# Performance work log

Hardware: AMD Instinct MI355X
Metric: run time of the kernel (lower is better)

Reference implementation:

```python
import jax, jax.numpy as jnp
import numpy as np

B, K, D, H, ZDIM = 65536, 16, 64, 128, 16

def setup_inputs() -> dict:
    key = jax.random.key(0)
    ks = jax.random.split(key, 20)
    s = 0.05
    inp = {
        'z': jax.random.normal(ks[0], (B, ZDIM), dtype=jnp.float32),
        'y': jax.random.randint(ks[1], (B,), 0, K),
        # backbone: 4 fc blocks (Linear+ReLU)
        'bw0': jax.random.normal(ks[2], (ZDIM, H), dtype=jnp.float32) * s,
        'bb0': jnp.zeros((H,), dtype=jnp.float32),
        'bw1': jax.random.normal(ks[3], (H, H), dtype=jnp.float32) * s,
        'bb1': jnp.zeros((H,), dtype=jnp.float32),
        'bw2': jax.random.normal(ks[4], (H, H), dtype=jnp.float32) * s,
        'bb2': jnp.zeros((H,), dtype=jnp.float32),
        'bw3': jax.random.normal(ks[5], (H, H), dtype=jnp.float32) * s,
        'bb3': jnp.zeros((H,), dtype=jnp.float32),
        # K heads, weights stacked on leading expert axis; layers 0-2 have ReLU, layer 3 does not
        'hw0': jax.random.normal(ks[6], (K, H, H), dtype=jnp.float32) * s,
        'hb0': jnp.zeros((K, H), dtype=jnp.float32),
        'hw1': jax.random.normal(ks[7], (K, H, H), dtype=jnp.float32) * s,
        'hb1': jnp.zeros((K, H), dtype=jnp.float32),
        'hw2': jax.random.normal(ks[8], (K, H, H), dtype=jnp.float32) * s,
        'hb2': jnp.zeros((K, H), dtype=jnp.float32),
        'hw3': jax.random.normal(ks[9], (K, H, D), dtype=jnp.float32) * s,
        'hb3': jnp.zeros((K, D), dtype=jnp.float32),
    }
    return inp

def reference(z, y, bw0, bb0, bw1, bb1, bw2, bb2, bw3, bb3,
              hw0, hb0, hw1, hb1, hw2, hb2, hw3, hb3):
    h = jax.nn.relu(z @ bw0 + bb0)
    h = jax.nn.relu(h @ bw1 + bb1)
    h = jax.nn.relu(h @ bw2 + bb2)
    h = jax.nn.relu(h @ bw3 + bb3)          # [B, H]
    # all K expert heads (faithful to original: compute all, then gather)
    a = jax.nn.relu(jnp.einsum('bi,kij->bkj', h, hw0) + hb0)  # [B, K, H]
    a = jax.nn.relu(jnp.einsum('bki,kij->bkj', a, hw1) + hb1)
    a = jax.nn.relu(jnp.einsum('bki,kij->bkj', a, hw2) + hb2)
    a = jnp.einsum('bki,kij->bkj', a, hw3) + hb3              # [B, K, D], no ReLU
    # select the y-th head per sample
    out = jnp.take_along_axis(a, y[:, None, None], axis=1)[:, 0, :]  # [B, D]
    return out
```

## Files before the change

### kernel.cpp

```cpp
#include <hip/hip_runtime.h>
#include <hip/hip_bf16.h>
#include <stdint.h>


typedef _Float16 f16;
typedef __attribute__((ext_vector_type(2)))  _Float16 f16x2;
typedef __attribute__((ext_vector_type(8)))  _Float16 f16x8;
typedef __attribute__((ext_vector_type(16))) float    f32x16;
typedef uint32_t u32;
typedef __attribute__((ext_vector_type(2))) u32 u32x2;
typedef __attribute__((ext_vector_type(4))) u32 u32x4;

#define MFMA(a, b, c) __builtin_amdgcn_mfma_f32_32x32x16_f16((a), (b), (c), 0, 0, 0)

constexpr int Bc = 65536;
constexpr int Kc = 16;
constexpr int Hc = 128;
constexpr int Dc = 64;

constexpr int CAP  = 4608;
constexpr int SPB  = 32;
constexpr int BPE  = CAP / SPB;
constexpr int NBLK = Kc * BPE;
constexpr int NXCD = 8;
constexpr int CHUNK = NBLK / NXCD;

constexpr int BBW_F16 = 2048 + 3 * 16384;
constexpr int HWE_F16 = 3 * 16384 + 8192;

constexpr int PREP_BLKS = 52 + Kc * 56;

struct Act { f16x8 w[8]; };

__device__ __forceinline__ f32x16 zero16() {
    f32x16 z;
#pragma unroll
    for (int i = 0; i < 16; ++i) z[i] = 0.0f;
    return z;
}

template<bool RELU>
__device__ __forceinline__ void build_windows(
    const f32x16& c, const float4* bq, f16x8& w0, f16x8& w1)
{
    u32 P[8];
#pragma unroll
    for (int g = 0; g < 4; ++g) {
        const float bb[4] = {bq[g].x, bq[g].y, bq[g].z, bq[g].w};
        f16 h[4];
#pragma unroll
        for (int j = 0; j < 4; ++j) {
            float v = c[4 * g + j] + bb[j];
            if (RELU) v = fmaxf(v, 0.0f);
            h[j] = (f16)v;
        }
        f16x2 p0; p0[0] = h[0]; p0[1] = h[1];
        f16x2 p1; p1[0] = h[2]; p1[1] = h[3];
        P[2 * g]     = __builtin_bit_cast(u32, p0);
        P[2 * g + 1] = __builtin_bit_cast(u32, p1);
    }
    const u32x2 r02 = __builtin_amdgcn_permlane32_swap(P[0], P[2], false, false);
    const u32x2 r13 = __builtin_amdgcn_permlane32_swap(P[1], P[3], false, false);
    const u32x2 r46 = __builtin_amdgcn_permlane32_swap(P[4], P[6], false, false);
    const u32x2 r57 = __builtin_amdgcn_permlane32_swap(P[5], P[7], false, false);
    u32x4 W0 = { r02[0], r13[0], r02[1], r13[1] };
    u32x4 W1 = { r46[0], r57[0], r46[1], r57[1] };
    w0 = __builtin_bit_cast(f16x8, W0);
    w1 = __builtin_bit_cast(f16x8, W1);
}

__device__ __forceinline__ void layer_glb(
    const f16* __restrict__ gW, const float* __restrict__ biasG,
    const Act& src, Act& dst, int lane, int bh)
{
#pragma unroll
    for (int q = 0; q < 4; ++q) {
        const f16* pw = gW + q * 4096 + lane * 8;
        float4 bq[4];
#pragma unroll
        for (int g = 0; g < 4; ++g)
            bq[g] = *(const float4*)(biasG + 32 * q + 8 * g + 4 * bh);

        f32x16 c0 = zero16(), c1 = zero16();
        __builtin_amdgcn_s_setprio(1);
#pragma unroll
        for (int ks = 0; ks < 8; ++ks) {
            const f16x8 wh = *(const f16x8*)(pw + ks * 512);
            if (ks & 1) c1 = MFMA(wh, src.w[ks], c1);
            else        c0 = MFMA(wh, src.w[ks], c0);
        }
        __builtin_amdgcn_s_setprio(0);
        const f32x16 cs = c0 + c1;
        build_windows<true>(cs, bq, dst.w[2 * q], dst.w[2 * q + 1]);
    }
}

__device__ __forceinline__ void layer_final(
    const f16* __restrict__ gW, const float* __restrict__ biasG,
    const Act& src, float* __restrict__ out, int bidx, int lane, int bh)
{
#pragma unroll
    for (int q = 0; q < 2; ++q) {
        const f16* pw = gW + q * 4096 + lane * 8;
        float4 bq[4];
#pragma unroll
        for (int g = 0; g < 4; ++g)
            bq[g] = *(const float4*)(biasG + 32 * q + 8 * g + 4 * bh);

        f32x16 c0 = zero16(), c1 = zero16();
        __builtin_amdgcn_s_setprio(1);
#pragma unroll
        for (int ks = 0; ks < 8; ++ks) {
            const f16x8 wh = *(const f16x8*)(pw + ks * 512);
            if (ks & 1) c1 = MFMA(wh, src.w[ks], c1);
            else        c0 = MFMA(wh, src.w[ks], c0);
        }
        __builtin_amdgcn_s_setprio(0);
        if (bidx >= 0) {
            const f32x16 cs = c0 + c1;
#pragma unroll
            for (int g = 0; g < 4; ++g) {
                float4 v;
                v.x = cs[4 * g + 0] + bq[g].x;
                v.y = cs[4 * g + 1] + bq[g].y;
                v.z = cs[4 * g + 2] + bq[g].z;
                v.w = cs[4 * g + 3] + bq[g].w;
                *(float4*)(out + (size_t)bidx * Dc + 32 * q + 8 * g + 4 * bh) = v;
            }
        }
    }
}

__global__ __launch_bounds__(64, 2) void fused_mlp(
    const float* __restrict__ z,
    const int* __restrict__ idxb, const int* __restrict__ cursor,
    const f16* __restrict__ bbW,
    const float* __restrict__ bb0, const float* __restrict__ bb1,
    const float* __restrict__ bb2, const float* __restrict__ bb3,
    const f16* __restrict__ hW,
    const float* __restrict__ hb0, const float* __restrict__ hb1,
    const float* __restrict__ hb2, const float* __restrict__ hb3,
    float* __restrict__ out)
{
    const int blk = (blockIdx.x % NXCD) * CHUNK + blockIdx.x / NXCD;
    const int e = blk / BPE;
    const int local0 = (blk % BPE) * SPB;
    const int cnt = min(cursor[e * 16], CAP);
    if (cnt - local0 <= 0) return;

    const int lane = threadIdx.x & 63;
    const int l31 = lane & 31, bh = lane >> 5;

    int bidx = -1;
    const int sIdx = local0 + l31;
    if (sIdx < cnt) bidx = idxb[e * CAP + sIdx];

    f16x8 zw;
    if (bidx >= 0) {
        const float4 u0 = *(const float4*)(z + (size_t)bidx * 16 + bh * 8);
        const float4 u1 = *(const float4*)(z + (size_t)bidx * 16 + bh * 8 + 4);
        zw[0] = (f16)u0.x; zw[1] = (f16)u0.y; zw[2] = (f16)u0.z; zw[3] = (f16)u0.w;
        zw[4] = (f16)u1.x; zw[5] = (f16)u1.y; zw[6] = (f16)u1.z; zw[7] = (f16)u1.w;
    } else {
#pragma unroll
        for (int j = 0; j < 8; ++j) zw[j] = (f16)0.0f;
    }

    Act aA, aB;
#pragma unroll
    for (int q = 0; q < 4; ++q) {
        float4 bq[4];
#pragma unroll
        for (int g = 0; g < 4; ++g)
            bq[g] = *(const float4*)(bb0 + 32 * q + 8 * g + 4 * bh);
        const f16x8 wh = *(const f16x8*)(bbW + q * 512 + lane * 8);
        f32x16 c0 = zero16();
        c0 = MFMA(wh, zw, c0);
        build_windows<true>(c0, bq, aA.w[2 * q], aA.w[2 * q + 1]);
    }

    const size_t we = (size_t)e * HWE_F16;
    layer_glb(bbW + 2048,      bb1,          aA, aB, lane, bh);
    layer_glb(bbW + 18432,     bb2,          aB, aA, lane, bh);
    layer_glb(bbW + 34816,     bb3,          aA, aB, lane, bh);
    layer_glb(hW + we,         hb0 + e * Hc, aB, aA, lane, bh);
    layer_glb(hW + we + 16384, hb1 + e * Hc, aA, aB, lane, bh);
    layer_glb(hW + we + 32768, hb2 + e * Hc, aB, aA, lane, bh);
    layer_final(hW + we + 49152, hb3 + e * Dc, aA, out, bidx, lane, bh);
}

__global__ void prep_scatter(
    const float* __restrict__ bw0, const float* __restrict__ bw1,
    const float* __restrict__ bw2, const float* __restrict__ bw3,
    const float* __restrict__ hw0, const float* __restrict__ hw1,
    const float* __restrict__ hw2, const float* __restrict__ hw3,
    f16* __restrict__ bbW, f16* __restrict__ hW,
    const int* __restrict__ y, int* __restrict__ idxb, int* __restrict__ cursor)
{
    __shared__ float T[32][33];
    __shared__ int lc[Kc];
    __shared__ int lbase[Kc];
    const int id = blockIdx.x;
    const int tx = threadIdx.x;

    if (id >= PREP_BLKS) {
        if (tx < Kc) lc[tx] = 0;
        __syncthreads();
        const int b = (id - PREP_BLKS) * 256 + tx;
        const int e = y[b];
        const int r = atomicAdd(&lc[e], 1);
        __syncthreads();
        if (tx < Kc) lbase[tx] = atomicAdd(&cursor[tx * 16], lc[tx]);
        __syncthreads();
        const int slot = lbase[e] + r;
        if (slot < CAP) idxb[e * CAP + slot] = b;
        return;
    }

    const float* src; f16 *dh;
    int K, N, k0, n0;
    bool big;

    if (id < 52) {
        if (id < 4) {
            src = bw0; dh = bbW;
            K = 16; N = 128; k0 = 0; n0 = id * 32; big = false;
        } else {
            const int t = id - 4;
            const int l = t / 16, tile = t % 16;
            const float* bws[3] = {bw1, bw2, bw3};
            src = bws[l];
            dh = bbW + 2048 + l * 16384;
            K = 128; N = 128; big = true;
            k0 = (tile >> 2) * 32; n0 = (tile & 3) * 32;
        }
    } else {
        const int t = id - 52;
        const int e = t / 56, r = t % 56;
        if (r < 48) {
            const int l = r / 16, tile = r % 16;
            const float* hws[3] = {hw0, hw1, hw2};
            src = hws[l] + (size_t)e * 16384;
            dh = hW + (size_t)e * HWE_F16 + l * 16384;
            K = 128; N = 128; big = true;
            k0 = (tile >> 2) * 32; n0 = (tile & 3) * 32;
        } else {
            const int r2 = r - 48;
            src = hw3 + (size_t)e * 8192;
            dh = hW + (size_t)e * HWE_F16 + 49152;
            K = 128; N = 64; big = true;
            k0 = (r2 >> 1) * 32; n0 = (r2 & 1) * 32;
        }
    }

    const int c = tx & 31, g = tx >> 5;
#pragma unroll
    for (int i = 0; i < 4; ++i) {
        const int row = g * 4 + i;
        if (k0 + row < K)
            T[c][row] = src[(size_t)(k0 + row) * N + n0 + c];
    }
    __syncthreads();
#pragma unroll
    for (int i = 0; i < 4; ++i) {
        const int n = n0 + g * 4 + i;
        const int k = k0 + c;
        if (k < K) {
            const float v = T[g * 4 + i][c];
            size_t didx;
            if (big)
                didx = (size_t)(n >> 5) * 4096 + (size_t)(k >> 4) * 512
                     + ((k >> 3) & 1) * 256 + (n & 31) * 8 + (k & 7);
            else
                didx = (size_t)(n >> 5) * 512 + (size_t)(k >> 3) * 256
                     + (n & 31) * 8 + (k & 7);
            dh[didx] = (f16)v;
        }
    }
}

extern "C" void kernel_launch(void* const* d_in, const int* in_sizes, int n_in,
                              void* d_out, int out_size, void* d_ws, size_t ws_size,
                              hipStream_t stream)
{
    const float* z   = (const float*)d_in[0];
    const int*   y   = (const int*)d_in[1];
    const float* bw0 = (const float*)d_in[2];
    const float* bb0 = (const float*)d_in[3];
    const float* bw1 = (const float*)d_in[4];
    const float* bb1 = (const float*)d_in[5];
    const float* bw2 = (const float*)d_in[6];
    const float* bb2 = (const float*)d_in[7];
    const float* bw3 = (const float*)d_in[8];
    const float* bb3 = (const float*)d_in[9];
    const float* hw0 = (const float*)d_in[10];
    const float* hb0 = (const float*)d_in[11];
    const float* hw1 = (const float*)d_in[12];
    const float* hb1 = (const float*)d_in[13];
    const float* hw2 = (const float*)d_in[14];
    const float* hb2 = (const float*)d_in[15];
    const float* hw3 = (const float*)d_in[16];
    const float* hb3 = (const float*)d_in[17];
    float* out = (float*)d_out;

    char* p = (char*)d_ws;
    f16* bbW = (f16*)p;  p += (size_t)BBW_F16 * 2;
    f16* hW  = (f16*)p;  p += (size_t)Kc * HWE_F16 * 2;
    int* idxb = (int*)p; p += (size_t)Kc * CAP * 4;
    int* cursor = (int*)p;

    hipMemsetAsync(cursor, 0, 256 * sizeof(int), stream);

    prep_scatter<<<PREP_BLKS + Bc / 256, 256, 0, stream>>>(
        bw0, bw1, bw2, bw3, hw0, hw1, hw2, hw3,
        bbW, hW, y, idxb, cursor);

    fused_mlp<<<NBLK, 64, 0, stream>>>(
        z, idxb, cursor, bbW, bb0, bb1, bb2, bb3,
        hW, hb0, hb1, hb2, hb3, out);
}
```

Measured before the change: 138.5 us.

## Double-buffer weight tiles in LDS via async global_load_lds prefetch

```diff
diff --git a/kernel.cpp b/kernel.cpp
--- a/kernel.cpp
+++ b/kernel.cpp
@@ -37,6 +37,23 @@
 #pragma unroll
     for (int i = 0; i < 16; ++i) z[i] = 0.0f;
     return z;
+}
+
+__device__ __forceinline__ void gload16(const f16* g, f16* l) {
+    __builtin_amdgcn_global_load_lds(
+        (const __attribute__((address_space(1))) void*)g,
+        (__attribute__((address_space(3))) void*)l, 16, 0, 0);
+}
+
+__device__ __forceinline__ void stage_q(f16* dst, const f16* gW, int lane) {
+#pragma unroll
+    for (int i = 0; i < 8; ++i)
+        gload16(gW + i * 512 + lane * 8, dst + i * 512);
+}
+
+__device__ __forceinline__ void pipe_wait() {
+    asm volatile("s_waitcnt vmcnt(8)" ::: "memory");
+    __builtin_amdgcn_sched_barrier(0);
 }
 
 template<bool RELU>
@@ -69,18 +86,21 @@
     w1 = __builtin_bit_cast(f16x8, W1);
 }
 
-__device__ __forceinline__ void layer_glb(
-    const f16* __restrict__ gW, const float* __restrict__ biasG,
-    const Act& src, Act& dst, int lane, int bh)
+__device__ __forceinline__ void layer_pipe(
+    f16* lds, const Act& src, Act& dst,
+    const f16* __restrict__ gW, const f16* __restrict__ gWN,
+    const float* __restrict__ biasG, int lane, int bh)
 {
 #pragma unroll
     for (int q = 0; q < 4; ++q) {
-        const f16* pw = gW + q * 4096 + lane * 8;
+        pipe_wait();
+
         float4 bq[4];
 #pragma unroll
         for (int g = 0; g < 4; ++g)
             bq[g] = *(const float4*)(biasG + 32 * q + 8 * g + 4 * bh);
 
+        const f16* pw = lds + (q & 1) * 4096 + lane * 8;
         f32x16 c0 = zero16(), c1 = zero16();
         __builtin_amdgcn_s_setprio(1);
 #pragma unroll
@@ -92,21 +112,27 @@
         __builtin_amdgcn_s_setprio(0);
         const f32x16 cs = c0 + c1;
         build_windows<true>(cs, bq, dst.w[2 * q], dst.w[2 * q + 1]);
+
+        __builtin_amdgcn_sched_barrier(0);
+        if (q < 2) stage_q(lds + (q & 1) * 4096, gW  + (q + 2) * 4096, lane);
+        else       stage_q(lds + (q & 1) * 4096, gWN + (q - 2) * 4096, lane);
     }
 }
 
 __device__ __forceinline__ void layer_final(
-    const f16* __restrict__ gW, const float* __restrict__ biasG,
-    const Act& src, float* __restrict__ out, int bidx, int lane, int bh)
+    const f16* lds, const Act& src, const float* __restrict__ biasG,
+    float* __restrict__ out, int bidx, int lane, int bh)
 {
 #pragma unroll
     for (int q = 0; q < 2; ++q) {
-        const f16* pw = gW + q * 4096 + lane * 8;
+        pipe_wait();
+
         float4 bq[4];
 #pragma unroll
         for (int g = 0; g < 4; ++g)
             bq[g] = *(const float4*)(biasG + 32 * q + 8 * g + 4 * bh);
 
+        const f16* pw = lds + (q & 1) * 4096 + lane * 8;
         f32x16 c0 = zero16(), c1 = zero16();
         __builtin_amdgcn_s_setprio(1);
 #pragma unroll
@@ -142,6 +168,8 @@
     const float* __restrict__ hb2, const float* __restrict__ hb3,
     float* __restrict__ out)
 {
+    __shared__ __attribute__((aligned(16))) f16 WLDS[2 * 4096];
+
     const int blk = (blockIdx.x % NXCD) * CHUNK + blockIdx.x / NXCD;
     const int e = blk / BPE;
     const int local0 = (blk % BPE) * SPB;
@@ -166,6 +194,9 @@
         for (int j = 0; j < 8; ++j) zw[j] = (f16)0.0f;
     }
 
+    stage_q(WLDS,        bbW + 2048,        lane);
+    stage_q(WLDS + 4096, bbW + 2048 + 4096, lane);
+
     Act aA, aB;
 #pragma unroll
     for (int q = 0; q < 4; ++q) {
@@ -180,13 +211,13 @@
     }
 
     const size_t we = (size_t)e * HWE_F16;
-    layer_glb(bbW + 2048,      bb1,          aA, aB, lane, bh);
-    layer_glb(bbW + 18432,     bb2,          aB, aA, lane, bh);
-    layer_glb(bbW + 34816,     bb3,          aA, aB, lane, bh);
-    layer_glb(hW + we,         hb0 + e * Hc, aB, aA, lane, bh);
-    layer_glb(hW + we + 16384, hb1 + e * Hc, aA, aB, lane, bh);
-    layer_glb(hW + we + 32768, hb2 + e * Hc, aB, aA, lane, bh);
-    layer_final(hW + we + 49152, hb3 + e * Dc, aA, out, bidx, lane, bh);
+    layer_pipe(WLDS, aA, aB, bbW + 2048,      bbW + 18432,     bb1, lane, bh);
+    layer_pipe(WLDS, aB, aA, bbW + 18432,     bbW + 34816,     bb2, lane, bh);
+    layer_pipe(WLDS, aA, aB, bbW + 34816,     hW + we,         bb3, lane, bh);
+    layer_pipe(WLDS, aB, aA, hW + we,         hW + we + 16384, hb0 + e * Hc, lane, bh);
+    layer_pipe(WLDS, aA, aB, hW + we + 16384, hW + we + 32768, hb1 + e * Hc, lane, bh);
+    layer_pipe(WLDS, aB, aA, hW + we + 32768, hW + we + 49152, hb2 + e * Hc, lane, bh);
+    layer_final(WLDS, aA, hb3 + e * Dc, out, bidx, lane, bh);
 }
 
 __global__ void prep_scatter(
```

Measured after the change: 130.8 us. -5.6%, faster.
